# Kernel tuning notes

Hardware: AMD Instinct MI355X
Metric: run time of the kernel (lower is better)

The kernel has to match this reference:

```python
import jax, jax.numpy as jnp
import numpy as np

B, H, S, D = 4, 16, 2048, 64
NEG = -1e9


def setup_inputs() -> dict:
    key = jax.random.key(0)
    kq, kk, kv, km = jax.random.split(key, 4)
    query = jax.random.normal(kq, (B, H, S, D), dtype=jnp.float32)
    k_ = jax.random.normal(kk, (B, H, S, D), dtype=jnp.float32)
    v_ = jax.random.normal(kv, (B, H, S, D), dtype=jnp.float32)
    mask = jax.random.randint(km, (B, S, S), 0, 2, dtype=jnp.int32)
    return {"query": query, "key": k_, "value": v_, "mask": mask}


def reference(query, key, value, mask):
    # scores: [B, H, S, S]
    scale = 1.0 / jnp.sqrt(jnp.asarray(query.shape[-1], query.dtype))
    scores = jnp.einsum('bhqd,bhkd->bhqk', query, key) * scale
    # mask [B,S,S] -> [B,1,S,S], broadcast over heads; masked_fill(mask==0, -1e9)
    scores = jnp.where(mask[:, None, :, :] == 0, jnp.asarray(NEG, scores.dtype), scores)
    attn = jax.nn.softmax(scores, axis=-1)
    return jnp.einsum('bhqk,bhkd->bhqd', attn, value)
```

## Files before the change

### kernel.cpp

```cpp
#include <hip/hip_runtime.h>
#include <stdint.h>


#define SQ 2048
#define DD 64

typedef __attribute__((ext_vector_type(8))) short short8;
typedef __attribute__((ext_vector_type(4))) short bshort4;
typedef __attribute__((ext_vector_type(4))) float f32x4;

union U8 { uint32_t u[4]; short8 s; };
union U4 { uint32_t u[2]; bshort4 s; };

__device__ __forceinline__ uint32_t pk_rne(float lo, float hi) {
  uint32_t a = __builtin_bit_cast(uint32_t, lo) + 0x8000u;
  uint32_t b = __builtin_bit_cast(uint32_t, hi) + 0x8000u;
  return __builtin_amdgcn_perm(b, a, 0x07060302u);
}
__device__ __forceinline__ uint32_t pk_tr(float lo, float hi) {
  return __builtin_amdgcn_perm(__builtin_bit_cast(uint32_t, hi),
                               __builtin_bit_cast(uint32_t, lo), 0x07060302u);
}

#if __has_builtin(__builtin_amdgcn_exp2f)
#define EXP2(x) __builtin_amdgcn_exp2f(x)
#else
#define EXP2(x) __exp2f(x)
#endif

__device__ __forceinline__ f32x4 mfma32(short8 a, short8 b, f32x4 c) {
  return __builtin_amdgcn_mfma_f32_16x16x32_bf16(a, b, c, 0, 0, 0);
}
#if __has_builtin(__builtin_amdgcn_mfma_f32_16x16x16bf16_1k)
__device__ __forceinline__ f32x4 mfma16(bshort4 a, bshort4 b, f32x4 c) {
  return __builtin_amdgcn_mfma_f32_16x16x16bf16_1k(a, b, c, 0, 0, 0);
}
#else
__device__ __forceinline__ f32x4 mfma16(bshort4 a, bshort4 b, f32x4 c) {
  asm("v_mfma_f32_16x16x16_bf16 %0, %1, %2, %0" : "+v"(c) : "v"(a), "v"(b));
  return c;
}
#endif

__device__ __forceinline__ void gload_lds16(const short* g, short* l) {
  __builtin_amdgcn_global_load_lds(
      (const __attribute__((address_space(1))) uint32_t*)g,
      (__attribute__((address_space(3))) uint32_t*)l, 16, 0, 0);
}

__global__ __launch_bounds__(256) void prep_all_kernel(
    const float* __restrict__ K, const float* __restrict__ V,
    const int* __restrict__ M, short* __restrict__ Kt,
    short* __restrict__ Vt, uint32_t* __restrict__ bits) {
  const int bid = blockIdx.x;
  if (bid < 4096) {
    int tid = bid * 256 + threadIdx.x;
    int l = tid & 63, rk = (tid >> 6) & 7, kt = (tid >> 9) & 31, bh = tid >> 14;
    int group = rk >> 2, sub = (rk >> 1) & 1, half = rk & 1;
    int i = l & 15;
    int key = kt * 64 + group * 32 + (i >> 2) * 8 + sub * 4 + (i & 3);
    int d0 = half * 32 + (l >> 4) * 8;
    const float* src = K + (size_t)bh * (SQ * DD) + (size_t)key * DD + d0;
    float4 a = ((const float4*)src)[0];
    float4 c = ((const float4*)src)[1];
    U8 w;
    w.u[0] = pk_rne(a.x, a.y); w.u[1] = pk_rne(a.z, a.w);
    w.u[2] = pk_rne(c.x, c.y); w.u[3] = pk_rne(c.z, c.w);
    *(short8*)(Kt + (size_t)tid * 8) = w.s;
  } else if (bid < 8192) {
    int tid = (bid - 4096) * 256 + threadIdx.x;
    int l = tid & 63, rv = (tid >> 6) & 7, kt = (tid >> 9) & 31, bh = tid >> 14;
    int group = rv >> 2, dc = rv & 3;
    int d = dc * 16 + (l & 15);
    int key0 = kt * 64 + group * 32 + (l >> 4) * 8;
    const float* s = V + (size_t)bh * (SQ * DD) + (size_t)key0 * DD + d;
    U8 w;
    w.u[0] = pk_rne(s[0], s[DD]);
    w.u[1] = pk_rne(s[2 * DD], s[3 * DD]);
    w.u[2] = pk_rne(s[4 * DD], s[5 * DD]);
    w.u[3] = pk_rne(s[6 * DD], s[7 * DD]);
    *(short8*)(Vt + (size_t)tid * 8) = w.s;
  } else {
    const int lane = threadIdx.x & 63;
    const int wid = ((bid - 8192) * 256 + threadIdx.x) >> 6;
    const int nw = (2048 * 256) >> 6;
    const size_t total = (size_t)4 * SQ * SQ;
    for (size_t base = (size_t)wid * 64; base < total; base += (size_t)nw * 64) {
      int v = M[base + lane];
      unsigned long long b = __ballot(v != 0);
      if (lane == 0) *(unsigned long long*)&bits[base >> 5] = b;
    }
  }
}

__global__ __launch_bounds__(256) void pack_mask_kernel(const int* __restrict__ m,
                                                        uint32_t* __restrict__ bits) {
  const int lane = threadIdx.x & 63;
  const int wid = (blockIdx.x * 256 + threadIdx.x) >> 6;
  const int nw = (gridDim.x * 256) >> 6;
  const size_t total = (size_t)4 * SQ * SQ;
  for (size_t base = (size_t)wid * 64; base < total; base += (size_t)nw * 64) {
    int v = m[base + lane];
    unsigned long long b = __ballot(v != 0);
    if (lane == 0) *(unsigned long long*)&bits[base >> 5] = b;
  }
}

__global__ __launch_bounds__(256, 4) void attn_fast(
    const float* __restrict__ Qg, const short* __restrict__ Kt,
    const short* __restrict__ Vt, const uint32_t* __restrict__ bits,
    float* __restrict__ Og) {
  __shared__ __align__(16) short sK[2][4096];
  __shared__ __align__(16) short sV[2][4096];
  __shared__ __align__(8) uint32_t sLut[32];

  const int tid = threadIdx.x;
  const int lane = tid & 63;
  const int wv = tid >> 6;
  const int l15 = lane & 15;
  const int quad = lane >> 4;

  const int bid = blockIdx.x;
  const int h = bid & 15;
  const int qt = (bid >> 4) & 15;
  const int b = bid >> 8;

  if (tid < 16) {
    uint32_t m0 = ((tid & 1) ? 0xFFFFu : 0u) | ((tid & 2) ? 0xFFFF0000u : 0u);
    uint32_t m1 = ((tid & 4) ? 0xFFFFu : 0u) | ((tid & 8) ? 0xFFFF0000u : 0u);
    sLut[tid * 2] = m0;
    sLut[tid * 2 + 1] = m1;
  }

  const size_t bh = (size_t)b * 16 + h;
  const float* Qp = Qg + bh * (size_t)(SQ * DD);
  const short* Kh = Kt + bh * (size_t)(SQ * DD);
  const short* Vh = Vt + bh * (size_t)(SQ * DD);
  float* Op = Og + bh * (size_t)(SQ * DD);
  const int q0w = qt * 128 + wv * 32;
  const int brow = b * SQ;

  const float QS = 0.18033688f;
  const float NC = -17.312340f;
  const f32x4 NCv = {NC, NC, NC, NC};

  U8 ones8u;
  ones8u.u[0] = 0x3f803f80u; ones8u.u[1] = 0x3f803f80u;
  ones8u.u[2] = 0x3f803f80u; ones8u.u[3] = 0x3f803f80u;
  const short8 ones8 = ones8u.s;

  short8 qf[2][2];
#pragma unroll
  for (int g = 0; g < 2; ++g)
#pragma unroll
    for (int dc = 0; dc < 2; ++dc) {
      const float* src = Qp + (size_t)(q0w + g * 16 + l15) * DD + dc * 32 + quad * 8;
      float4 a = *(const float4*)src;
      float4 c = *(const float4*)(src + 4);
      U8 t;
      t.u[0] = pk_rne(a.x * QS, a.y * QS);
      t.u[1] = pk_rne(a.z * QS, a.w * QS);
      t.u[2] = pk_rne(c.x * QS, c.y * QS);
      t.u[3] = pk_rne(c.z * QS, c.w * QS);
      qf[g][dc] = t.s;
    }

  f32x4 o[2][4];
  f32x4 osum[2];
#pragma unroll
  for (int g = 0; g < 2; ++g) {
#pragma unroll
    for (int dc = 0; dc < 4; ++dc) o[g][dc] = (f32x4){0.f, 0.f, 0.f, 0.f};
    osum[g] = (f32x4){0.f, 0.f, 0.f, 0.f};
  }

  const int rk0 = wv * 2, rk1 = wv * 2 + 1;
  const short* kg0 = Kh + rk0 * 512 + lane * 8;
  const short* kg1 = Kh + rk1 * 512 + lane * 8;
  const short* vg0 = Vh + rk0 * 512 + lane * 8;
  const short* vg1 = Vh + rk1 * 512 + lane * 8;

  uint2 mwc[2], mwn[2];
#pragma unroll
  for (int g = 0; g < 2; ++g)
    mwc[g] = *(const uint2*)&bits[(size_t)(brow + q0w + g * 16 + l15) * (SQ / 32)];

  gload_lds16(kg0, &sK[0][rk0 * 512]);
  gload_lds16(kg1, &sK[0][rk1 * 512]);
  gload_lds16(vg0, &sV[0][rk0 * 512]);
  gload_lds16(vg1, &sV[0][rk1 * 512]);

  const int shA = quad * 8;
  const int shB = quad * 8 + 4;

  for (int kt = 0; kt < SQ / 64; ++kt) {
    const int buf = kt & 1;

    __syncthreads();

    if (kt + 1 < SQ / 64) {
      const int off = (kt + 1) * 4096;
      gload_lds16(kg0 + off, &sK[buf ^ 1][rk0 * 512]);
      gload_lds16(kg1 + off, &sK[buf ^ 1][rk1 * 512]);
      gload_lds16(vg0 + off, &sV[buf ^ 1][rk0 * 512]);
      gload_lds16(vg1 + off, &sV[buf ^ 1][rk1 * 512]);
#pragma unroll
      for (int g = 0; g < 2; ++g)
        mwn[g] = *(const uint2*)&bits[(size_t)(brow + q0w + g * 16 + l15) * (SQ / 32) + (kt + 1) * 2];
    }

    const short* kb_base = &sK[buf][lane * 8];
    const short* vb_base = &sV[buf][lane * 8];

#pragma unroll
    for (int grp = 0; grp < 2; ++grp) {
      short8 kA0 = *(const short8*)&kb_base[(grp * 4 + 0) * 512];
      short8 kA1 = *(const short8*)&kb_base[(grp * 4 + 1) * 512];
      short8 kB0 = *(const short8*)&kb_base[(grp * 4 + 2) * 512];
      short8 kB1 = *(const short8*)&kb_base[(grp * 4 + 3) * 512];
      short8 vf[4];
#pragma unroll
      for (int dc = 0; dc < 4; ++dc)
        vf[dc] = *(const short8*)&vb_base[(grp * 4 + dc) * 512];

#pragma unroll
      for (int g = 0; g < 2; ++g) {
        uint32_t w = grp ? mwc[g].y : mwc[g].x;
        uint32_t tA = (w >> shA) & 15u;
        uint32_t tB = (w >> shB) & 15u;
        uint2 mskA = *(const uint2*)&sLut[tA * 2];
        uint2 mskB = *(const uint2*)&sLut[tB * 2];
        __builtin_amdgcn_s_setprio(1);
        f32x4 stA = mfma32(kA0, qf[g][0], NCv);
        stA = mfma32(kA1, qf[g][1], stA);
        f32x4 stB = mfma32(kB0, qf[g][0], NCv);
        stB = mfma32(kB1, qf[g][1], stB);
        __builtin_amdgcn_s_setprio(0);
        float pA0 = EXP2(stA[0]), pA1 = EXP2(stA[1]);
        float pA2 = EXP2(stA[2]), pA3 = EXP2(stA[3]);
        float pB0 = EXP2(stB[0]), pB1 = EXP2(stB[1]);
        float pB2 = EXP2(stB[2]), pB3 = EXP2(stB[3]);
        U8 pw;
        pw.u[0] = pk_tr(pA0, pA1) & mskA.x;
        pw.u[1] = pk_tr(pA2, pA3) & mskA.y;
        pw.u[2] = pk_tr(pB0, pB1) & mskB.x;
        pw.u[3] = pk_tr(pB2, pB3) & mskB.y;
        __builtin_amdgcn_s_setprio(1);
#pragma unroll
        for (int dc = 0; dc < 4; ++dc)
          o[g][dc] = mfma32(pw.s, vf[dc], o[g][dc]);
        osum[g] = mfma32(pw.s, ones8, osum[g]);
        __builtin_amdgcn_s_setprio(0);
      }
    }

    if (kt + 1 < SQ / 64) {
#pragma unroll
      for (int g = 0; g < 2; ++g) mwc[g] = mwn[g];
    }
  }

#pragma unroll
  for (int g = 0; g < 2; ++g)
#pragma unroll
    for (int r = 0; r < 4; ++r) {
      float inv = 1.0f / osum[g][r];
      float* dst = Op + (size_t)(q0w + g * 16 + quad * 4 + r) * DD + l15;
      dst[0]  = o[g][0][r] * inv;
      dst[16] = o[g][1][r] * inv;
      dst[32] = o[g][2][r] * inv;
      dst[48] = o[g][3][r] * inv;
    }
}

template <bool USE_BITS>
__global__ __launch_bounds__(256, 2) void attn_fb(
    const float* __restrict__ Qg, const float* __restrict__ Kg,
    const float* __restrict__ Vg, const int* __restrict__ Mg,
    const uint32_t* __restrict__ bits, float* __restrict__ Og) {
  __shared__ __align__(16) short sK[2][64 * 72];
  __shared__ __align__(16) short sVT[2][64 * 72];
  const int tid = threadIdx.x;
  const int lane = tid & 63;
  const int wv = tid >> 6;
  const int l15 = lane & 15;
  const int quad = lane >> 4;
  const int bid = blockIdx.x;
  const int h = bid & 15;
  const int qt = (bid >> 4) & 7;
  const int b = bid >> 7;
  const size_t bh = (size_t)b * 16 + h;
  const float* Qp = Qg + bh * (size_t)(SQ * DD);
  const float* Kp = Kg + bh * (size_t)(SQ * DD);
  const float* Vp = Vg + bh * (size_t)(SQ * DD);
  float* Op = Og + bh * (size_t)(SQ * DD);
  const int q0w = qt * 256 + wv * 64;
  const int brow = b * SQ;
  const float QS = 0.18033688f, NC = -17.312340f;
  const float NINF = -__builtin_inff();
  U4 onesu; onesu.u[0] = 0x3f803f80u; onesu.u[1] = 0x3f803f80u;
  const bshort4 ones = onesu.s;
  short8 qf[4][2];
#pragma unroll
  for (int g = 0; g < 4; ++g)
#pragma unroll
    for (int dc = 0; dc < 2; ++dc) {
      const float* src = Qp + (size_t)(q0w + g * 16 + l15) * DD + dc * 32 + quad * 8;
      float4 a = *(const float4*)src;
      float4 c = *(const float4*)(src + 4);
      U8 t;
      t.u[0] = pk_rne(a.x * QS, a.y * QS); t.u[1] = pk_rne(a.z * QS, a.w * QS);
      t.u[2] = pk_rne(c.x * QS, c.y * QS); t.u[3] = pk_rne(c.z * QS, c.w * QS);
      qf[g][dc] = t.s;
    }
  f32x4 o[4][4]; f32x4 osum[4];
#pragma unroll
  for (int g = 0; g < 4; ++g) {
#pragma unroll
    for (int dc = 0; dc < 4; ++dc) o[g][dc] = (f32x4){0.f, 0.f, 0.f, 0.f};
    osum[g] = (f32x4){0.f, 0.f, 0.f, 0.f};
  }
  const int kr = lane, kcb = wv * 16;
  const int vr2 = (lane & 31) * 2, vcb = wv * 16 + (lane >> 5) * 8;
  const float* kbase = Kp + (size_t)kr * DD + kcb;
  const float* vbase = Vp + (size_t)vr2 * DD + vcb;
  float4 kA, kB, kC, kD, vA, vB, vC, vD;
  uint2 mwc[4], mwn[4];
  {
    const float4* kp = (const float4*)kbase;
    kA = kp[0]; kB = kp[1]; kC = kp[2]; kD = kp[3];
    const float* r0 = vbase;
    vA = ((const float4*)r0)[0]; vB = ((const float4*)r0)[1];
    vC = ((const float4*)(r0 + DD))[0]; vD = ((const float4*)(r0 + DD))[1];
    if (USE_BITS) {
#pragma unroll
      for (int g = 0; g < 4; ++g)
        mwc[g] = *(const uint2*)&bits[(size_t)(brow + q0w + g * 16 + l15) * (SQ / 32)];
    }
    U8 w0, w1;
    w0.u[0] = pk_rne(kA.x, kA.y); w0.u[1] = pk_rne(kA.z, kA.w);
    w0.u[2] = pk_rne(kB.x, kB.y); w0.u[3] = pk_rne(kB.z, kB.w);
    w1.u[0] = pk_rne(kC.x, kC.y); w1.u[1] = pk_rne(kC.z, kC.w);
    w1.u[2] = pk_rne(kD.x, kD.y); w1.u[3] = pk_rne(kD.z, kD.w);
    *(short8*)&sK[0][kr * 72 + kcb] = w0.s;
    *(short8*)&sK[0][kr * 72 + kcb + 8] = w1.s;
    float av[8] = {vA.x, vA.y, vA.z, vA.w, vB.x, vB.y, vB.z, vB.w};
    float bv[8] = {vC.x, vC.y, vC.z, vC.w, vD.x, vD.y, vD.z, vD.w};
#pragma unroll
    for (int j = 0; j < 8; ++j)
      *(uint32_t*)&sVT[0][(vcb + j) * 72 + vr2] = pk_rne(av[j], bv[j]);
  }
  for (int kt = 0; kt < SQ / 64; ++kt) {
    const int buf = kt & 1;
    const int k0 = kt * 64;
    __syncthreads();
    if (kt + 1 < SQ / 64) {
      const float4* kp = (const float4*)(kbase + (size_t)(k0 + 64) * DD);
      kA = kp[0]; kB = kp[1]; kC = kp[2]; kD = kp[3];
      const float* r0 = vbase + (size_t)(k0 + 64) * DD;
      vA = ((const float4*)r0)[0]; vB = ((const float4*)r0)[1];
      vC = ((const float4*)(r0 + DD))[0]; vD = ((const float4*)(r0 + DD))[1];
      if (USE_BITS) {
#pragma unroll
        for (int g = 0; g < 4; ++g)
          mwn[g] = *(const uint2*)&bits[(size_t)(brow + q0w + g * 16 + l15) * (SQ / 32) + (kt + 1) * 2];
      }
    }
    const short* sKb = sK[buf];
    const short* sVb = sVT[buf];
#pragma unroll
    for (int kb = 0; kb < 4; ++kb) {
      short8 kfa = *(const short8*)&sKb[(kb * 16 + l15) * 72 + quad * 8];
      short8 kfb = *(const short8*)&sKb[(kb * 16 + l15) * 72 + 32 + quad * 8];
      bshort4 vf[4];
#pragma unroll
      for (int dc = 0; dc < 4; ++dc)
        vf[dc] = *(const bshort4*)&sVb[(dc * 16 + l15) * 72 + kb * 16 + quad * 4];
#pragma unroll
      for (int g = 0; g < 4; ++g) {
        uint32_t t;
        if (USE_BITS) {
          uint32_t w = (kb & 2) ? mwc[g].y : mwc[g].x;
          t = w >> ((kb & 1) * 16 + quad * 4);
        } else {
          const int* mrow = Mg + (size_t)(brow + q0w + g * 16 + l15) * SQ + k0 + kb * 16 + quad * 4;
          t = (mrow[0] != 0) | ((mrow[1] != 0) << 1) | ((mrow[2] != 0) << 2) |
              ((mrow[3] != 0) << 3);
        }
        f32x4 ci;
        ci[0] = (t & 1) ? NC : NINF;
        ci[1] = (t & 2) ? NC : NINF;
        ci[2] = (t & 4) ? NC : NINF;
        ci[3] = (t & 8) ? NC : NINF;
        f32x4 st = mfma32(kfa, qf[g][0], ci);
        st = mfma32(kfb, qf[g][1], st);
        float p0 = EXP2(st[0]), p1 = EXP2(st[1]), p2 = EXP2(st[2]), p3 = EXP2(st[3]);
        U4 pw;
        pw.u[0] = pk_tr(p0, p1);
        pw.u[1] = pk_tr(p2, p3);
#pragma unroll
        for (int dc = 0; dc < 4; ++dc)
          o[g][dc] = mfma16(pw.s, vf[dc], o[g][dc]);
        osum[g] = mfma16(pw.s, ones, osum[g]);
      }
    }
    if (kt + 1 < SQ / 64) {
      short* dK = (short*)sK[buf ^ 1];
      short* dV = (short*)sVT[buf ^ 1];
      U8 w0, w1;
      w0.u[0] = pk_rne(kA.x, kA.y); w0.u[1] = pk_rne(kA.z, kA.w);
      w0.u[2] = pk_rne(kB.x, kB.y); w0.u[3] = pk_rne(kB.z, kB.w);
      w1.u[0] = pk_rne(kC.x, kC.y); w1.u[1] = pk_rne(kC.z, kC.w);
      w1.u[2] = pk_rne(kD.x, kD.y); w1.u[3] = pk_rne(kD.z, kD.w);
      *(short8*)&dK[kr * 72 + kcb] = w0.s;
      *(short8*)&dK[kr * 72 + kcb + 8] = w1.s;
      float av[8] = {vA.x, vA.y, vA.z, vA.w, vB.x, vB.y, vB.z, vB.w};
      float bv[8] = {vC.x, vC.y, vC.z, vC.w, vD.x, vD.y, vD.z, vD.w};
#pragma unroll
      for (int j = 0; j < 8; ++j)
        *(uint32_t*)&dV[(vcb + j) * 72 + vr2] = pk_rne(av[j], bv[j]);
      if (USE_BITS) {
#pragma unroll
        for (int g = 0; g < 4; ++g) mwc[g] = mwn[g];
      }
    }
  }
#pragma unroll
  for (int g = 0; g < 4; ++g)
#pragma unroll
    for (int r = 0; r < 4; ++r) {
      float inv = 1.0f / osum[g][r];
      float* dst = Op + (size_t)(q0w + g * 16 + quad * 4 + r) * DD + l15;
      dst[0]  = o[g][0][r] * inv;
      dst[16] = o[g][1][r] * inv;
      dst[32] = o[g][2][r] * inv;
      dst[48] = o[g][3][r] * inv;
    }
}

extern "C" void kernel_launch(void* const* d_in, const int* in_sizes, int n_in,
                              void* d_out, int out_size, void* d_ws, size_t ws_size,
                              hipStream_t stream) {
  const float* Q = (const float*)d_in[0];
  const float* K = (const float*)d_in[1];
  const float* V = (const float*)d_in[2];
  const int* M = (const int*)d_in[3];
  float* out = (float*)d_out;

  const size_t bits_bytes = (size_t)4 * SQ * SQ / 8;
  const size_t kv_bytes = (size_t)64 * SQ * DD * 2;
  const size_t full_bytes = bits_bytes + 2 * kv_bytes;

  if (ws_size >= full_bytes) {
    uint32_t* bits = (uint32_t*)d_ws;
    short* Kt = (short*)((char*)d_ws + bits_bytes);
    short* Vt = (short*)((char*)d_ws + bits_bytes + kv_bytes);
    prep_all_kernel<<<10240, 256, 0, stream>>>(K, V, M, Kt, Vt, bits);
    attn_fast<<<4 * (SQ / 128) * 16, 256, 0, stream>>>(Q, Kt, Vt, bits, out);
  } else if (ws_size >= bits_bytes) {
    uint32_t* bits = (uint32_t*)d_ws;
    pack_mask_kernel<<<2048, 256, 0, stream>>>(M, bits);
    attn_fb<true><<<4 * (SQ / 256) * 16, 256, 0, stream>>>(Q, K, V, M, bits, out);
  } else {
    attn_fb<false><<<4 * (SQ / 256) * 16, 256, 0, stream>>>(Q, K, V, M, nullptr, out);
  }
}
```

Measured before the change: 264.7 us.

## Stage K/V conversion through LDS tiles and compute mask lanes in registers

The K/V bf16 repack in the prep kernel now loads each 64x64 tile coalesced into padded shared memory. Each thread then gathers its fragment from LDS instead of doing strided global reads, which matters most for V's column-wise access. Each block now handles a whole tile, so the grid shrinks from 10240 to 6144 blocks. Separately, the attention kernel drops its shared-memory mask lookup table and builds the 16-bit lane masks from the mask bits with ALU ops, removing LDS reads from the inner loop at the cost of a few extra VALU instructions.

After: 397.0 us. 50.0% more time.

```diff
diff --git a/kernel.cpp b/kernel.cpp
--- a/kernel.cpp
+++ b/kernel.cpp
@@ -48,41 +48,67 @@
       (__attribute__((address_space(3))) uint32_t*)l, 16, 0, 0);
 }
 
+#define LSTR 66
+
 __global__ __launch_bounds__(256) void prep_all_kernel(
     const float* __restrict__ K, const float* __restrict__ V,
     const int* __restrict__ M, short* __restrict__ Kt,
     short* __restrict__ Vt, uint32_t* __restrict__ bits) {
+  __shared__ float sT[64 * LSTR];
   const int bid = blockIdx.x;
+  const int t = threadIdx.x;
+
   if (bid < 4096) {
-    int tid = bid * 256 + threadIdx.x;
-    int l = tid & 63, rk = (tid >> 6) & 7, kt = (tid >> 9) & 31, bh = tid >> 14;
-    int group = rk >> 2, sub = (rk >> 1) & 1, half = rk & 1;
-    int i = l & 15;
-    int key = kt * 64 + group * 32 + (i >> 2) * 8 + sub * 4 + (i & 3);
-    int d0 = half * 32 + (l >> 4) * 8;
-    const float* src = K + (size_t)bh * (SQ * DD) + (size_t)key * DD + d0;
-    float4 a = ((const float4*)src)[0];
-    float4 c = ((const float4*)src)[1];
-    U8 w;
-    w.u[0] = pk_rne(a.x, a.y); w.u[1] = pk_rne(a.z, a.w);
-    w.u[2] = pk_rne(c.x, c.y); w.u[3] = pk_rne(c.z, c.w);
-    *(short8*)(Kt + (size_t)tid * 8) = w.s;
-  } else if (bid < 8192) {
-    int tid = (bid - 4096) * 256 + threadIdx.x;
-    int l = tid & 63, rv = (tid >> 6) & 7, kt = (tid >> 9) & 31, bh = tid >> 14;
-    int group = rv >> 2, dc = rv & 3;
-    int d = dc * 16 + (l & 15);
-    int key0 = kt * 64 + group * 32 + (l >> 4) * 8;
-    const float* s = V + (size_t)bh * (SQ * DD) + (size_t)key0 * DD + d;
-    U8 w;
-    w.u[0] = pk_rne(s[0], s[DD]);
-    w.u[1] = pk_rne(s[2 * DD], s[3 * DD]);
-    w.u[2] = pk_rne(s[4 * DD], s[5 * DD]);
-    w.u[3] = pk_rne(s[6 * DD], s[7 * DD]);
-    *(short8*)(Vt + (size_t)tid * 8) = w.s;
+    const int tile = bid & 2047;
+    const bool isK = bid < 2048;
+    const float* src = (isK ? K : V) +
+                       (size_t)(tile >> 5) * (SQ * DD) + (size_t)(tile & 31) * 4096;
+#pragma unroll
+    for (int p = 0; p < 8; ++p) {
+      int row = (t >> 5) + p * 8;
+      int c2 = (t & 31) * 2;
+      float2 v = *(const float2*)(src + row * 64 + c2);
+      sT[row * LSTR + c2] = v.x;
+      sT[row * LSTR + c2 + 1] = v.y;
+    }
+    __syncthreads();
+
+    const int l = t & 63;
+    if (isK) {
+      short* dst = Kt + (size_t)tile * 4096;
+#pragma unroll
+      for (int half8 = 0; half8 < 2; ++half8) {
+        int rk = (t >> 6) + half8 * 4;
+        int group = rk >> 2, sub = (rk >> 1) & 1, half = rk & 1;
+        int i = l & 15;
+        int keyl = group * 32 + (i >> 2) * 8 + sub * 4 + (i & 3);
+        int d0 = half * 32 + (l >> 4) * 8;
+        const float* s = &sT[keyl * LSTR + d0];
+        U8 w;
+        w.u[0] = pk_rne(s[0], s[1]); w.u[1] = pk_rne(s[2], s[3]);
+        w.u[2] = pk_rne(s[4], s[5]); w.u[3] = pk_rne(s[6], s[7]);
+        *(short8*)(dst + (rk * 64 + l) * 8) = w.s;
+      }
+    } else {
+      short* dst = Vt + (size_t)tile * 4096;
+#pragma unroll
+      for (int half8 = 0; half8 < 2; ++half8) {
+        int rv = (t >> 6) + half8 * 4;
+        int group = rv >> 2, dc = rv & 3;
+        int d = dc * 16 + (l & 15);
+        int k0 = group * 32 + (l >> 4) * 8;
+        const float* s = &sT[k0 * LSTR + d];
+        U8 w;
+        w.u[0] = pk_rne(s[0 * LSTR], s[1 * LSTR]);
+        w.u[1] = pk_rne(s[2 * LSTR], s[3 * LSTR]);
+        w.u[2] = pk_rne(s[4 * LSTR], s[5 * LSTR]);
+        w.u[3] = pk_rne(s[6 * LSTR], s[7 * LSTR]);
+        *(short8*)(dst + (rv * 64 + l) * 8) = w.s;
+      }
+    }
   } else {
-    const int lane = threadIdx.x & 63;
-    const int wid = ((bid - 8192) * 256 + threadIdx.x) >> 6;
+    const int lane = t & 63;
+    const int wid = ((bid - 4096) * 256 + t) >> 6;
     const int nw = (2048 * 256) >> 6;
     const size_t total = (size_t)4 * SQ * SQ;
     for (size_t base = (size_t)wid * 64; base < total; base += (size_t)nw * 64) {
@@ -112,7 +138,6 @@
     float* __restrict__ Og) {
   __shared__ __align__(16) short sK[2][4096];
   __shared__ __align__(16) short sV[2][4096];
-  __shared__ __align__(8) uint32_t sLut[32];
 
   const int tid = threadIdx.x;
   const int lane = tid & 63;
@@ -124,13 +149,6 @@
   const int h = bid & 15;
   const int qt = (bid >> 4) & 15;
   const int b = bid >> 8;
-
-  if (tid < 16) {
-    uint32_t m0 = ((tid & 1) ? 0xFFFFu : 0u) | ((tid & 2) ? 0xFFFF0000u : 0u);
-    uint32_t m1 = ((tid & 4) ? 0xFFFFu : 0u) | ((tid & 8) ? 0xFFFF0000u : 0u);
-    sLut[tid * 2] = m0;
-    sLut[tid * 2 + 1] = m1;
-  }
 
   const size_t bh = (size_t)b * 16 + h;
   const float* Qp = Qg + bh * (size_t)(SQ * DD);
@@ -228,8 +246,10 @@
         uint32_t w = grp ? mwc[g].y : mwc[g].x;
         uint32_t tA = (w >> shA) & 15u;
         uint32_t tB = (w >> shB) & 15u;
-        uint2 mskA = *(const uint2*)&sLut[tA * 2];
-        uint2 mskB = *(const uint2*)&sLut[tB * 2];
+        uint32_t mA0 = ((tA & 1u) ? 0xFFFFu : 0u) | ((tA & 2u) ? 0xFFFF0000u : 0u);
+        uint32_t mA1 = ((tA & 4u) ? 0xFFFFu : 0u) | ((tA & 8u) ? 0xFFFF0000u : 0u);
+        uint32_t mB0 = ((tB & 1u) ? 0xFFFFu : 0u) | ((tB & 2u) ? 0xFFFF0000u : 0u);
+        uint32_t mB1 = ((tB & 4u) ? 0xFFFFu : 0u) | ((tB & 8u) ? 0xFFFF0000u : 0u);
         __builtin_amdgcn_s_setprio(1);
         f32x4 stA = mfma32(kA0, qf[g][0], NCv);
         stA = mfma32(kA1, qf[g][1], stA);
@@ -241,10 +261,10 @@
         float pB0 = EXP2(stB[0]), pB1 = EXP2(stB[1]);
         float pB2 = EXP2(stB[2]), pB3 = EXP2(stB[3]);
         U8 pw;
-        pw.u[0] = pk_tr(pA0, pA1) & mskA.x;
-        pw.u[1] = pk_tr(pA2, pA3) & mskA.y;
-        pw.u[2] = pk_tr(pB0, pB1) & mskB.x;
-        pw.u[3] = pk_tr(pB2, pB3) & mskB.y;
+        pw.u[0] = pk_tr(pA0, pA1) & mA0;
+        pw.u[1] = pk_tr(pA2, pA3) & mA1;
+        pw.u[2] = pk_tr(pB0, pB1) & mB0;
+        pw.u[3] = pk_tr(pB2, pB3) & mB1;
         __builtin_amdgcn_s_setprio(1);
 #pragma unroll
         for (int dc = 0; dc < 4; ++dc)
@@ -455,7 +475,7 @@
     uint32_t* bits = (uint32_t*)d_ws;
     short* Kt = (short*)((char*)d_ws + bits_bytes);
     short* Vt = (short*)((char*)d_ws + bits_bytes + kv_bytes);
-    prep_all_kernel<<<10240, 256, 0, stream>>>(K, V, M, Kt, Vt, bits);
+    prep_all_kernel<<<6144, 256, 0, stream>>>(K, V, M, Kt, Vt, bits);
     attn_fast<<<4 * (SQ / 128) * 16, 256, 0, stream>>>(Q, Kt, Vt, bits, out);
   } else if (ws_size >= bits_bytes) {
     uint32_t* bits = (uint32_t*)d_ws;
```
